# Performance work log

Hardware: AMD Instinct MI355X
Metric: run time of the kernel (lower is better)

Reference implementation:

```python
import jax, jax.numpy as jnp
import numpy as np

N = 50000
E = 800000
IN_DIM = 512
HID = 256
LAT = 128
K = 10
ALPHA = 0.1
BN_EPS = 1e-5


def setup_inputs() -> dict:
    key = jax.random.key(0)
    ks = jax.random.split(key, 6)
    x = jax.random.normal(ks[0], (N, IN_DIM), dtype=jnp.float32)
    edge_index = jax.random.randint(ks[1], (2, E), 0, N, dtype=jnp.int64)
    W_proj = jax.random.normal(ks[2], (IN_DIM, LAT), dtype=jnp.float32) * (IN_DIM ** -0.5)
    W1 = jax.random.normal(ks[3], (LAT, HID), dtype=jnp.float32) * (LAT ** -0.5)
    W2 = jax.random.normal(ks[4], (HID, LAT), dtype=jnp.float32) * (HID ** -0.5)
    return {
        "x": x, "edge_index": edge_index, "W_proj": W_proj,
        "W1": W1, "b1": jnp.zeros((HID,), jnp.float32),
        "gamma1": jnp.ones((HID,), jnp.float32), "beta1": jnp.zeros((HID,), jnp.float32),
        "mean1": jnp.zeros((HID,), jnp.float32), "var1": jnp.ones((HID,), jnp.float32),
        "W2": W2, "b2": jnp.zeros((LAT,), jnp.float32),
        "gamma2": jnp.ones((LAT,), jnp.float32), "beta2": jnp.zeros((LAT,), jnp.float32),
        "mean2": jnp.zeros((LAT,), jnp.float32), "var2": jnp.ones((LAT,), jnp.float32),
    }


def _gcn_norm(edge_index, n):
    # add self-loops, symmetric normalization D^-1/2 A D^-1/2 (PyG gcn_norm)
    loops = jnp.arange(n, dtype=edge_index.dtype)
    src = jnp.concatenate([edge_index[0], loops])
    dst = jnp.concatenate([edge_index[1], loops])
    deg = jax.ops.segment_sum(jnp.ones_like(dst, jnp.float32), dst, num_segments=n)
    dinv = jax.lax.rsqrt(jnp.maximum(deg, 1.0))  # deg >= 1 with self-loops
    norm = dinv[src] * dinv[dst]
    return src, dst, norm


def _propagate(h, src, dst, norm, n):
    # gather -> scale -> scatter-add: out[dst] += norm * h[src]
    return jax.ops.segment_sum(h[src] * norm[:, None], dst, num_segments=n)


def _bn(h, gamma, beta, mean, var):
    # BatchNorm1d in eval mode (running stats)
    return (h - mean) * jax.lax.rsqrt(var + BN_EPS) * gamma + beta


def reference(x, edge_index, W_proj, W1, b1, gamma1, beta1, mean1, var1,
              W2, b2, gamma2, beta2, mean2, var2):
    n = x.shape[0]
    src, dst, norm = _gcn_norm(edge_index, n)

    z0 = x @ W_proj                                   # [N, LAT]
    h1 = _propagate(z0 @ W1, src, dst, norm, n) + b1  # GCNConv 1
    h1 = jax.nn.relu(_bn(h1, gamma1, beta1, mean1, var1))
    h2 = _propagate(h1 @ W2, src, dst, norm, n) + b2  # GCNConv 2
    h2 = jax.nn.relu(_bn(h2, gamma2, beta2, mean2, var2))

    # APPNP: h_k = (1-alpha) * A_hat h_{k-1} + alpha * h_0
    def step(h, _):
        h = (1.0 - ALPHA) * _propagate(h, src, dst, norm, n) + ALPHA * h2
        return h, None
    z_refined, _ = jax.lax.scan(step, h2, None, length=K)

    z = z_refined + z0
    row, col = edge_index[0], edge_index[1]
    adj = jax.nn.sigmoid(jnp.sum(z[row] * z[col], axis=1))  # [E]
    return adj, z
```

## Files before the change

kernel.cpp:

```cpp
#include <hip/hip_runtime.h>

#define N_NODES 50000
#define N_EDGES 800000
#define IN_DIM  512
#define HID     256
#define LAT     128
#define K_ITERS 10
#define BN_EPS  1e-5f

typedef __attribute__((ext_vector_type(8))) short bf16x8;
typedef __attribute__((ext_vector_type(4))) float f32x4;

__device__ inline float bflo(unsigned v) { return __builtin_bit_cast(float, v << 16); }
__device__ inline float bfhi(unsigned v) { return __builtin_bit_cast(float, v & 0xffff0000u); }
__device__ inline unsigned f2bf_bits(float f)
{
    unsigned u = __builtin_bit_cast(unsigned, f);
    return (u + 0x7fffu + ((u >> 16) & 1u)) >> 16;
}
__device__ inline unsigned packbf(float x, float y)
{
    return f2bf_bits(x) | (f2bf_bits(y) << 16);
}

__global__ void detect_dtype_kernel(const int* __restrict__ ei32, int* __restrict__ flag)
{
    __shared__ int any;
    if (threadIdx.x == 0) any = 0;
    __syncthreads();
    int local = 0;
    for (int i = threadIdx.x; i < 4096; i += blockDim.x)
        local |= ei32[2 * i + 1];
    if (local) atomicOr(&any, 1);
    __syncthreads();
    if (threadIdx.x == 0) flag[0] = (any != 0) ? 1 : 0;
}

__global__ void init_cnt_kernel(int* __restrict__ cnt, int n)
{
    int i = blockIdx.x * blockDim.x + threadIdx.x;
    if (i < n) cnt[i] = 1;
}

__global__ void convert_count_kernel(const void* __restrict__ ei, const int* __restrict__ flag,
                                     int* __restrict__ srcE, int* __restrict__ dstE,
                                     int* __restrict__ cnt, int E)
{
    int e = blockIdx.x * blockDim.x + threadIdx.x;
    if (e >= E) return;
    int s, d;
    if (*flag) {
        const int* p = (const int*)ei;
        s = p[e]; d = p[E + e];
    } else {
        const long long* p = (const long long*)ei;
        s = (int)p[e]; d = (int)p[E + e];
    }
    srcE[e] = s;
    dstE[e] = d;
    atomicAdd(&cnt[d], 1);
}

__global__ __launch_bounds__(256) void block_sum_kernel(const int* __restrict__ cnt,
                                                        int* __restrict__ bsum, int n)
{
    __shared__ int s[256];
    int i = blockIdx.x * 256 + threadIdx.x;
    s[threadIdx.x] = (i < n) ? cnt[i] : 0;
    __syncthreads();
    for (int off = 128; off > 0; off >>= 1) {
        if (threadIdx.x < off) s[threadIdx.x] += s[threadIdx.x + off];
        __syncthreads();
    }
    if (threadIdx.x == 0) bsum[blockIdx.x] = s[0];
}

__global__ __launch_bounds__(256) void block_scan_kernel(int* __restrict__ bsum, int nb)
{
    __shared__ int s[256];
    int t = threadIdx.x;
    int v = (t < nb) ? bsum[t] : 0;
    s[t] = v;
    __syncthreads();
    for (int off = 1; off < 256; off <<= 1) {
        int u = (t >= off) ? s[t - off] : 0;
        __syncthreads();
        s[t] += u;
        __syncthreads();
    }
    if (t < nb) bsum[t] = s[t] - v;
}

__global__ __launch_bounds__(256) void final_scan_kernel(const int* __restrict__ cnt,
                                                         const int* __restrict__ bsum,
                                                         int* __restrict__ rowoff,
                                                         int* __restrict__ cursor,
                                                         float* __restrict__ dinv, int n)
{
    __shared__ int s[256];
    int t = threadIdx.x;
    int i = blockIdx.x * 256 + t;
    int c = (i < n) ? cnt[i] : 0;
    s[t] = c;
    __syncthreads();
    for (int off = 1; off < 256; off <<= 1) {
        int u = (t >= off) ? s[t - off] : 0;
        __syncthreads();
        s[t] += u;
        __syncthreads();
    }
    if (i < n) {
        int excl = bsum[blockIdx.x] + s[t] - c;
        rowoff[i] = excl;
        cursor[i] = excl;
        dinv[i] = rsqrtf((float)c);
    }
    if (i == 0) rowoff[n] = N_EDGES + N_NODES;
}

__global__ void scatter_kernel(const int* __restrict__ srcE, const int* __restrict__ dstE,
                               const float* __restrict__ dinv, int* __restrict__ cursor,
                               uint2* __restrict__ csr, int E, int n)
{
    int e = blockIdx.x * blockDim.x + threadIdx.x;
    if (e >= E + n) return;
    int s, d;
    if (e < E) { s = srcE[e]; d = dstE[e]; }
    else       { s = e - E;   d = s; }
    int pos = atomicAdd(&cursor[d], 1);
    float w = dinv[s] * dinv[d];
    csr[pos] = make_uint2((unsigned)s, __builtin_bit_cast(unsigned, w));
}

__global__ void transpose_cvt_kernel(const float* __restrict__ in, unsigned short* __restrict__ out,
                                     int R, int C)
{
    int idx = blockIdx.x * 256 + threadIdx.x;
    if (idx >= R * C) return;
    int c = idx / R, r = idx - c * R;
    out[idx] = (unsigned short)f2bf_bits(in[r * C + c]);
}

template<int KDIM, int EPI, bool AF32>
__global__ __launch_bounds__(256) void gemm_pipe(const void* __restrict__ Ain,
                                                 const unsigned short* __restrict__ Bt,
                                                 unsigned short* __restrict__ Cout,
                                                 int M, int Nc,
                                                 const float* __restrict__ cb,
                                                 const float* __restrict__ cg,
                                                 const float* __restrict__ cbe,
                                                 const float* __restrict__ cm,
                                                 const float* __restrict__ cv)
{
    constexpr int NK = KDIM / 32;
    constexpr int PREF = AF32 ? (NK < 4 ? NK : 4) : (NK < 8 ? NK : 8);
    const int wave = threadIdx.x >> 6;
    const int lane = threadIdx.x & 63;
    const int s  = lane & 15;
    const int kc = lane >> 4;
    const int wrow0   = blockIdx.y * 64 + wave * 16;
    const int colbase = blockIdx.x * 128;
    int arow = wrow0 + s; if (arow > M - 1) arow = M - 1;

    const float*          Af = (const float*)Ain + (size_t)arow * KDIM + 8 * kc;
    const unsigned short* Ah = (const unsigned short*)Ain + (size_t)arow * KDIM + 8 * kc;
    const unsigned short* Bp = Bt + (size_t)(colbase + s) * KDIM + 8 * kc;

    float4 Araw[AF32 ? PREF : 1][2];
    bf16x8 Areg[AF32 ? 1 : PREF];
    bf16x8 Breg[2][8];
    f32x4  acc[8] = {};

#pragma unroll
    for (int i = 0; i < PREF; ++i) {
        if constexpr (AF32) {
            Araw[i][0] = *(const float4*)(Af + 32 * i);
            Araw[i][1] = *(const float4*)(Af + 32 * i + 4);
        } else {
            Areg[i] = *(const bf16x8*)(Ah + 32 * i);
        }
    }
#pragma unroll
    for (int t = 0; t < 8; ++t)
        Breg[0][t] = *(const bf16x8*)(Bp + (size_t)16 * t * KDIM);

#pragma unroll
    for (int k = 0; k < NK; ++k) {
        if (k + 1 < NK) {
#pragma unroll
            for (int t = 0; t < 8; ++t)
                Breg[(k + 1) & 1][t] = *(const bf16x8*)(Bp + (size_t)16 * t * KDIM + 32 * (k + 1));
        }
        bf16x8 af;
        if constexpr (AF32) {
            float4 u0 = Araw[k % PREF][0];
            float4 u1 = Araw[k % PREF][1];
            if (k + PREF < NK) {
                Araw[k % PREF][0] = *(const float4*)(Af + 32 * (k + PREF));
                Araw[k % PREF][1] = *(const float4*)(Af + 32 * (k + PREF) + 4);
            }
            af[0] = (short)f2bf_bits(u0.x); af[1] = (short)f2bf_bits(u0.y);
            af[2] = (short)f2bf_bits(u0.z); af[3] = (short)f2bf_bits(u0.w);
            af[4] = (short)f2bf_bits(u1.x); af[5] = (short)f2bf_bits(u1.y);
            af[6] = (short)f2bf_bits(u1.z); af[7] = (short)f2bf_bits(u1.w);
        } else {
            af = Areg[k % PREF];
            if (k + PREF < NK)
                Areg[k % PREF] = *(const bf16x8*)(Ah + 32 * (k + PREF));
        }
#pragma unroll
        for (int t = 0; t < 8; ++t)
            acc[t] = __builtin_amdgcn_mfma_f32_16x16x32_bf16(af, Breg[k & 1][t], acc[t], 0, 0, 0);
    }

#pragma unroll
    for (int t = 0; t < 8; ++t) {
        const int col = colbase + t * 16 + s;
        float sc = 1.f, sh = 0.f;
        if (EPI == 1) {
            sc = cg[col] * rsqrtf(cv[col] + BN_EPS);
            sh = (cb[col] - cm[col]) * sc + cbe[col];
        }
#pragma unroll
        for (int j = 0; j < 4; ++j) {
            const int crow = wrow0 + kc * 4 + j;
            if (crow < M) {
                float xv = acc[t][j];
                if (EPI == 1) xv = fmaxf(fmaf(xv, sc, sh), 0.f);
                Cout[(size_t)crow * Nc + col] = (unsigned short)f2bf_bits(xv);
            }
        }
    }
}

template<int MODE>
__global__ __launch_bounds__(256) void prop_row(const unsigned* __restrict__ in,
                                                const int* __restrict__ rowoff,
                                                const unsigned long long* __restrict__ csr,
                                                const unsigned* __restrict__ h2h,
                                                const unsigned* __restrict__ z0h,
                                                float* __restrict__ outf,
                                                unsigned* __restrict__ outh,
                                                const float* __restrict__ bb,
                                                const float* __restrict__ bg,
                                                const float* __restrict__ bbe,
                                                const float* __restrict__ bm,
                                                const float* __restrict__ bv)
{
    const int node = blockIdx.x * 4 + (threadIdx.x >> 6);
    const int lane = threadIdx.x & 63;
    const int g = lane >> 4, s = lane & 15;
    const int e0 = rowoff[node], e1 = rowoff[node + 1];

    float f[8] = {};
    int e = e0 + g;
    while (e < e1) {
        unsigned long long P[6];
        uint4 V[6];
#pragma unroll
        for (int i = 0; i < 6; ++i) { P[i] = 0; V[i] = make_uint4(0u, 0u, 0u, 0u); }
#pragma unroll
        for (int i = 0; i < 6; ++i)
            if (e + 4 * i < e1) P[i] = csr[e + 4 * i];
#pragma unroll
        for (int i = 0; i < 6; ++i)
            if (e + 4 * i < e1) V[i] = *(const uint4*)&in[(size_t)(unsigned)P[i] * 64 + 4 * s];
#pragma unroll
        for (int i = 0; i < 6; ++i) {
            const float w = __builtin_bit_cast(float, (unsigned)(P[i] >> 32));
            f[0] = fmaf(w, bflo(V[i].x), f[0]); f[1] = fmaf(w, bfhi(V[i].x), f[1]);
            f[2] = fmaf(w, bflo(V[i].y), f[2]); f[3] = fmaf(w, bfhi(V[i].y), f[3]);
            f[4] = fmaf(w, bflo(V[i].z), f[4]); f[5] = fmaf(w, bfhi(V[i].z), f[5]);
            f[6] = fmaf(w, bflo(V[i].w), f[6]); f[7] = fmaf(w, bfhi(V[i].w), f[7]);
        }
        e += 24;
    }
#pragma unroll
    for (int i = 0; i < 8; ++i) {
        f[i] += __shfl_xor(f[i], 16, 64);
        f[i] += __shfl_xor(f[i], 32, 64);
    }

    if (g == 0) {
        const size_t o = (size_t)node * 64 + 4 * s;
        uint4 ov;
        if (MODE == 0) {
            ov.x = packbf(f[0], f[1]); ov.y = packbf(f[2], f[3]);
            ov.z = packbf(f[4], f[5]); ov.w = packbf(f[6], f[7]);
            *(uint4*)&outh[o] = ov;
        } else if (MODE == 1) {
            float4 G0 = *(const float4*)&bg[8 * s],  G1 = *(const float4*)&bg[8 * s + 4];
            float4 V0 = *(const float4*)&bv[8 * s],  V1 = *(const float4*)&bv[8 * s + 4];
            float4 B0 = *(const float4*)&bb[8 * s],  B1 = *(const float4*)&bb[8 * s + 4];
            float4 M0 = *(const float4*)&bm[8 * s],  M1 = *(const float4*)&bm[8 * s + 4];
            float4 E0 = *(const float4*)&bbe[8 * s], E1 = *(const float4*)&bbe[8 * s + 4];
            float gg[8] = {G0.x, G0.y, G0.z, G0.w, G1.x, G1.y, G1.z, G1.w};
            float vv[8] = {V0.x, V0.y, V0.z, V0.w, V1.x, V1.y, V1.z, V1.w};
            float bbv[8] = {B0.x, B0.y, B0.z, B0.w, B1.x, B1.y, B1.z, B1.w};
            float mm[8] = {M0.x, M0.y, M0.z, M0.w, M1.x, M1.y, M1.z, M1.w};
            float ee[8] = {E0.x, E0.y, E0.z, E0.w, E1.x, E1.y, E1.z, E1.w};
            float r[8];
#pragma unroll
            for (int i = 0; i < 8; ++i) {
                float sc = gg[i] * rsqrtf(vv[i] + BN_EPS);
                float sh = (bbv[i] - mm[i]) * sc + ee[i];
                r[i] = fmaxf(fmaf(f[i], sc, sh), 0.f);
            }
            ov.x = packbf(r[0], r[1]); ov.y = packbf(r[2], r[3]);
            ov.z = packbf(r[4], r[5]); ov.w = packbf(r[6], r[7]);
            *(uint4*)&outh[o] = ov;
        } else if (MODE == 2) {
            uint4 hv = *(const uint4*)&h2h[o];
            ov.x = packbf(fmaf(0.9f, f[0], 0.1f * bflo(hv.x)), fmaf(0.9f, f[1], 0.1f * bfhi(hv.x)));
            ov.y = packbf(fmaf(0.9f, f[2], 0.1f * bflo(hv.y)), fmaf(0.9f, f[3], 0.1f * bfhi(hv.y)));
            ov.z = packbf(fmaf(0.9f, f[4], 0.1f * bflo(hv.z)), fmaf(0.9f, f[5], 0.1f * bfhi(hv.z)));
            ov.w = packbf(fmaf(0.9f, f[6], 0.1f * bflo(hv.w)), fmaf(0.9f, f[7], 0.1f * bfhi(hv.w)));
            *(uint4*)&outh[o] = ov;
        } else {
            uint4 hv = *(const uint4*)&h2h[o];
            uint4 zv = *(const uint4*)&z0h[o];
            float r[8];
            r[0] = fmaf(0.9f, f[0], 0.1f * bflo(hv.x)) + bflo(zv.x);
            r[1] = fmaf(0.9f, f[1], 0.1f * bfhi(hv.x)) + bfhi(zv.x);
            r[2] = fmaf(0.9f, f[2], 0.1f * bflo(hv.y)) + bflo(zv.y);
            r[3] = fmaf(0.9f, f[3], 0.1f * bfhi(hv.y)) + bfhi(zv.y);
            r[4] = fmaf(0.9f, f[4], 0.1f * bflo(hv.z)) + bflo(zv.z);
            r[5] = fmaf(0.9f, f[5], 0.1f * bfhi(hv.z)) + bfhi(zv.z);
            r[6] = fmaf(0.9f, f[6], 0.1f * bflo(hv.w)) + bflo(zv.w);
            r[7] = fmaf(0.9f, f[7], 0.1f * bfhi(hv.w)) + bfhi(zv.w);
            *(float4*)&outf[(size_t)node * LAT + 8 * s]     = make_float4(r[0], r[1], r[2], r[3]);
            *(float4*)&outf[(size_t)node * LAT + 8 * s + 4] = make_float4(r[4], r[5], r[6], r[7]);
            ov.x = packbf(r[0], r[1]); ov.y = packbf(r[2], r[3]);
            ov.z = packbf(r[4], r[5]); ov.w = packbf(r[6], r[7]);
            *(uint4*)&outh[o] = ov;
        }
    }
}

__global__ __launch_bounds__(256) void edge_dot_mfma(const unsigned* __restrict__ zh,
                                                     const int* __restrict__ srcE,
                                                     const int* __restrict__ dstE,
                                                     float* __restrict__ adj)
{
    const int gw = blockIdx.x * 4 + (threadIdx.x >> 6);
    const int base = gw * 16;
    const int lane = threadIdx.x & 63;
    const int s = lane & 15, kc = lane >> 4;
    const int r = srcE[base + s];
    const int c = dstE[base + s];
    const unsigned* zr = &zh[(size_t)r * 64 + 4 * kc];
    const unsigned* zc = &zh[(size_t)c * 64 + 4 * kc];
    f32x4 acc = {};
#pragma unroll
    for (int k0 = 0; k0 < 4; ++k0) {
        bf16x8 af = *(const bf16x8*)(zr + 16 * k0);
        bf16x8 bf = *(const bf16x8*)(zc + 16 * k0);
        acc = __builtin_amdgcn_mfma_f32_16x16x32_bf16(af, bf, acc, 0, 0, 0);
    }
    if ((s >> 2) == kc) {
        const int j = s & 3;
        float v = (j == 0) ? acc[0] : (j == 1) ? acc[1] : (j == 2) ? acc[2] : acc[3];
        adj[base + s] = 1.f / (1.f + expf(-v));
    }
}

extern "C" void kernel_launch(void* const* d_in, const int* in_sizes, int n_in,
                              void* d_out, int out_size, void* d_ws, size_t ws_size,
                              hipStream_t stream)
{
    const float* x     = (const float*)d_in[0];
    const void*  ei    = d_in[1];
    const float* Wproj = (const float*)d_in[2];
    const float* W1    = (const float*)d_in[3];
    const float* b1    = (const float*)d_in[4];
    const float* g1    = (const float*)d_in[5];
    const float* be1   = (const float*)d_in[6];
    const float* m1    = (const float*)d_in[7];
    const float* v1    = (const float*)d_in[8];
    const float* W2    = (const float*)d_in[9];
    const float* b2    = (const float*)d_in[10];
    const float* g2    = (const float*)d_in[11];
    const float* be2   = (const float*)d_in[12];
    const float* m2    = (const float*)d_in[13];
    const float* v2    = (const float*)d_in[14];

    float* out_adj = (float*)d_out;
    float* out_z   = (float*)d_out + N_EDGES;

    char* w = (char*)d_ws;
    size_t off = 0;
    auto alloc = [&](size_t bytes) {
        void* p = w + off;
        off += (bytes + 255) & ~(size_t)255;
        return p;
    };
    const size_t NB = (size_t)N_NODES * 64 * 4;
    const int NBLK = (N_NODES + 255) / 256;

    int*            flag   = (int*)           alloc(4);
    int*            cnt    = (int*)           alloc((size_t)N_NODES * 4);
    int*            cursor = (int*)           alloc((size_t)N_NODES * 4);
    int*            rowoff = (int*)           alloc((size_t)(N_NODES + 1) * 4);
    float*          dinv   = (float*)         alloc((size_t)N_NODES * 4);
    int*            bsum   = (int*)           alloc(256 * 4);
    int*            srcE   = (int*)           alloc((size_t)N_EDGES * 4);
    int*            dstE   = (int*)           alloc((size_t)N_EDGES * 4);
    uint2*          csr    = (uint2*)         alloc((size_t)(N_EDGES + N_NODES) * 8);
    unsigned short* Wpt    = (unsigned short*)alloc((size_t)LAT * IN_DIM * 2);
    unsigned short* W1t    = (unsigned short*)alloc((size_t)HID * LAT * 2);
    unsigned short* W2t    = (unsigned short*)alloc((size_t)LAT * HID * 2);
    unsigned*       z0h    = (unsigned*)      alloc(NB);
    unsigned*       p0h    = (unsigned*)      alloc(NB);
    unsigned short* h1h    = (unsigned short*)alloc(2 * NB);
    unsigned*       t2h    = (unsigned*)      alloc(NB);
    unsigned*       h2h    = (unsigned*)      alloc(NB);

    unsigned* pingA = (unsigned*)h1h;
    unsigned* pingB = (unsigned*)h1h + N_NODES * 64;

    detect_dtype_kernel<<<1, 256, 0, stream>>>((const int*)ei, flag);
    init_cnt_kernel<<<(N_NODES + 255) / 256, 256, 0, stream>>>(cnt, N_NODES);
    convert_count_kernel<<<(N_EDGES + 255) / 256, 256, 0, stream>>>(ei, flag, srcE, dstE, cnt, N_EDGES);
    block_sum_kernel<<<NBLK, 256, 0, stream>>>(cnt, bsum, N_NODES);
    block_scan_kernel<<<1, 256, 0, stream>>>(bsum, NBLK);
    final_scan_kernel<<<NBLK, 256, 0, stream>>>(cnt, bsum, rowoff, cursor, dinv, N_NODES);
    scatter_kernel<<<(N_EDGES + N_NODES + 255) / 256, 256, 0, stream>>>(srcE, dstE, dinv, cursor,
                                                                        csr, N_EDGES, N_NODES);

    transpose_cvt_kernel<<<(IN_DIM * LAT + 255) / 256, 256, 0, stream>>>(Wproj, Wpt, IN_DIM, LAT);
    transpose_cvt_kernel<<<(LAT * HID + 255) / 256, 256, 0, stream>>>(W1, W1t, LAT, HID);
    transpose_cvt_kernel<<<(HID * LAT + 255) / 256, 256, 0, stream>>>(W2, W2t, HID, LAT);

    const int gy = (N_NODES + 63) / 64;
    const int pgrid = N_NODES / 4;

    gemm_pipe<IN_DIM, 0, true><<<dim3(1, gy), 256, 0, stream>>>(x, Wpt, (unsigned short*)z0h,
                                                                N_NODES, LAT,
                                                                nullptr, nullptr, nullptr, nullptr, nullptr);
    prop_row<0><<<pgrid, 256, 0, stream>>>(z0h, rowoff, (const unsigned long long*)csr,
                                           nullptr, nullptr, nullptr, p0h,
                                           nullptr, nullptr, nullptr, nullptr, nullptr);
    gemm_pipe<LAT, 1, false><<<dim3(2, gy), 256, 0, stream>>>(p0h, W1t, h1h, N_NODES, HID,
                                                              b1, g1, be1, m1, v1);
    gemm_pipe<HID, 0, false><<<dim3(1, gy), 256, 0, stream>>>(h1h, W2t, (unsigned short*)t2h,
                                                              N_NODES, LAT,
                                                              nullptr, nullptr, nullptr, nullptr, nullptr);
    prop_row<1><<<pgrid, 256, 0, stream>>>(t2h, rowoff, (const unsigned long long*)csr,
                                           nullptr, nullptr, nullptr, h2h,
                                           b2, g2, be2, m2, v2);

    const unsigned* cur = h2h;
    for (int it = 0; it < K_ITERS; ++it) {
        if (it == K_ITERS - 1) {
            prop_row<3><<<pgrid, 256, 0, stream>>>(cur, rowoff, (const unsigned long long*)csr,
                                                   h2h, z0h, out_z, z0h,
                                                   nullptr, nullptr, nullptr, nullptr, nullptr);
        } else {
            unsigned* nxt = (it & 1) ? pingB : pingA;
            prop_row<2><<<pgrid, 256, 0, stream>>>(cur, rowoff, (const unsigned long long*)csr,
                                                   h2h, nullptr, nullptr, nxt,
                                                   nullptr, nullptr, nullptr, nullptr, nullptr);
            cur = nxt;
        }
    }

    edge_dot_mfma<<<N_EDGES / 64, 256, 0, stream>>>(z0h, srcE, dstE, out_adj);
}
```

Baseline: 719.7 us.

## Stage weight tiles in LDS for GEMMs with MFMA-friendly pre-tiled layout

The GEMM kernels now stage 64-deep chunks of the weight matrix into shared memory with a register double-buffered prefetch, so B is read once per block instead of every wave reading it from global memory. The weight transpose kernel writes a tiled layout that lets each thread copy contiguous 64-byte runs and lets the MFMA operand reads come straight from LDS. This targets redundant global/L2 traffic for B in the dense projections. In exchange it adds block-wide barriers per chunk and LDS bank-access patterns that may reduce overlap.

```diff
diff --git a/kernel.cpp b/kernel.cpp
--- a/kernel.cpp
+++ b/kernel.cpp
@@ -132,85 +132,107 @@
     csr[pos] = make_uint2((unsigned)s, __builtin_bit_cast(unsigned, w));
 }
 
-__global__ void transpose_cvt_kernel(const float* __restrict__ in, unsigned short* __restrict__ out,
-                                     int R, int C)
+__global__ void transpose_cvt_tile(const float* __restrict__ in, unsigned short* __restrict__ out,
+                                   int K, int C)
 {
     int idx = blockIdx.x * 256 + threadIdx.x;
-    if (idx >= R * C) return;
-    int c = idx / R, r = idx - c * R;
-    out[idx] = (unsigned short)f2bf_bits(in[r * C + c]);
+    if (idx >= K * C) return;
+    int k = idx / C, col = idx - k * C;
+    int dst = (col >> 7) * (K * 128) + (k >> 3) * 1024 + ((col & 127) << 3) + (k & 7);
+    out[dst] = (unsigned short)f2bf_bits(in[idx]);
 }
 
 template<int KDIM, int EPI, bool AF32>
-__global__ __launch_bounds__(256) void gemm_pipe(const void* __restrict__ Ain,
-                                                 const unsigned short* __restrict__ Bt,
-                                                 unsigned short* __restrict__ Cout,
-                                                 int M, int Nc,
-                                                 const float* __restrict__ cb,
-                                                 const float* __restrict__ cg,
-                                                 const float* __restrict__ cbe,
-                                                 const float* __restrict__ cm,
-                                                 const float* __restrict__ cv)
-{
-    constexpr int NK = KDIM / 32;
-    constexpr int PREF = AF32 ? (NK < 4 ? NK : 4) : (NK < 8 ? NK : 8);
-    const int wave = threadIdx.x >> 6;
-    const int lane = threadIdx.x & 63;
+__global__ __launch_bounds__(256) void gemm_lds(const void* __restrict__ Ain,
+                                                const unsigned short* __restrict__ Bt,
+                                                unsigned short* __restrict__ Cout,
+                                                int M, int Nc,
+                                                const float* __restrict__ cb,
+                                                const float* __restrict__ cg,
+                                                const float* __restrict__ cbe,
+                                                const float* __restrict__ cm,
+                                                const float* __restrict__ cv)
+{
+    constexpr int BK = 64;
+    constexpr int NC = KDIM / BK;
+    __shared__ unsigned short Bl[BK * 128];
+    const int tid  = threadIdx.x;
+    const int wave = tid >> 6;
+    const int lane = tid & 63;
     const int s  = lane & 15;
     const int kc = lane >> 4;
     const int wrow0   = blockIdx.y * 64 + wave * 16;
     const int colbase = blockIdx.x * 128;
     int arow = wrow0 + s; if (arow > M - 1) arow = M - 1;
 
-    const float*          Af = (const float*)Ain + (size_t)arow * KDIM + 8 * kc;
-    const unsigned short* Ah = (const unsigned short*)Ain + (size_t)arow * KDIM + 8 * kc;
-    const unsigned short* Bp = Bt + (size_t)(colbase + s) * KDIM + 8 * kc;
-
-    float4 Araw[AF32 ? PREF : 1][2];
-    bf16x8 Areg[AF32 ? 1 : PREF];
-    bf16x8 Breg[2][8];
+    const float*          Af   = (const float*)Ain + (size_t)arow * KDIM + 8 * kc;
+    const unsigned short* Ahp  = (const unsigned short*)Ain + (size_t)arow * KDIM + 8 * kc;
+    const unsigned short* Bblk = Bt + (size_t)blockIdx.x * KDIM * 128;
+
+    float4 Arf[2][2][2];
+    bf16x8 Arh[2][2];
+    uint4  Bst[4];
     f32x4  acc[8] = {};
 
-#pragma unroll
-    for (int i = 0; i < PREF; ++i) {
+    {
+        const uint4* src = (const uint4*)(Bblk + tid * 32);
+        Bst[0] = src[0]; Bst[1] = src[1]; Bst[2] = src[2]; Bst[3] = src[3];
+    }
+#pragma unroll
+    for (int kk = 0; kk < 2; ++kk) {
         if constexpr (AF32) {
-            Araw[i][0] = *(const float4*)(Af + 32 * i);
-            Araw[i][1] = *(const float4*)(Af + 32 * i + 4);
+            Arf[0][kk][0] = *(const float4*)(Af + 32 * kk);
+            Arf[0][kk][1] = *(const float4*)(Af + 32 * kk + 4);
         } else {
-            Areg[i] = *(const bf16x8*)(Ah + 32 * i);
-        }
-    }
-#pragma unroll
-    for (int t = 0; t < 8; ++t)
-        Breg[0][t] = *(const bf16x8*)(Bp + (size_t)16 * t * KDIM);
-
-#pragma unroll
-    for (int k = 0; k < NK; ++k) {
-        if (k + 1 < NK) {
-#pragma unroll
-            for (int t = 0; t < 8; ++t)
-                Breg[(k + 1) & 1][t] = *(const bf16x8*)(Bp + (size_t)16 * t * KDIM + 32 * (k + 1));
-        }
-        bf16x8 af;
-        if constexpr (AF32) {
-            float4 u0 = Araw[k % PREF][0];
-            float4 u1 = Araw[k % PREF][1];
-            if (k + PREF < NK) {
-                Araw[k % PREF][0] = *(const float4*)(Af + 32 * (k + PREF));
-                Araw[k % PREF][1] = *(const float4*)(Af + 32 * (k + PREF) + 4);
+            Arh[0][kk] = *(const bf16x8*)(Ahp + 32 * kk);
+        }
+    }
+    {
+        uint4* d = (uint4*)&Bl[tid * 32];
+        d[0] = Bst[0]; d[1] = Bst[1]; d[2] = Bst[2]; d[3] = Bst[3];
+    }
+    __syncthreads();
+
+#pragma unroll
+    for (int c = 0; c < NC; ++c) {
+        if (c + 1 < NC) {
+            const uint4* src = (const uint4*)(Bblk + (c + 1) * 8192 + tid * 32);
+            Bst[0] = src[0]; Bst[1] = src[1]; Bst[2] = src[2]; Bst[3] = src[3];
+#pragma unroll
+            for (int kk = 0; kk < 2; ++kk) {
+                if constexpr (AF32) {
+                    Arf[(c + 1) & 1][kk][0] = *(const float4*)(Af + (c + 1) * 64 + 32 * kk);
+                    Arf[(c + 1) & 1][kk][1] = *(const float4*)(Af + (c + 1) * 64 + 32 * kk + 4);
+                } else {
+                    Arh[(c + 1) & 1][kk] = *(const bf16x8*)(Ahp + (c + 1) * 64 + 32 * kk);
+                }
             }
-            af[0] = (short)f2bf_bits(u0.x); af[1] = (short)f2bf_bits(u0.y);
-            af[2] = (short)f2bf_bits(u0.z); af[3] = (short)f2bf_bits(u0.w);
-            af[4] = (short)f2bf_bits(u1.x); af[5] = (short)f2bf_bits(u1.y);
-            af[6] = (short)f2bf_bits(u1.z); af[7] = (short)f2bf_bits(u1.w);
-        } else {
-            af = Areg[k % PREF];
-            if (k + PREF < NK)
-                Areg[k % PREF] = *(const bf16x8*)(Ah + 32 * (k + PREF));
-        }
-#pragma unroll
-        for (int t = 0; t < 8; ++t)
-            acc[t] = __builtin_amdgcn_mfma_f32_16x16x32_bf16(af, Breg[k & 1][t], acc[t], 0, 0, 0);
+        }
+#pragma unroll
+        for (int kk = 0; kk < 2; ++kk) {
+            bf16x8 af;
+            if constexpr (AF32) {
+                float4 u0 = Arf[c & 1][kk][0];
+                float4 u1 = Arf[c & 1][kk][1];
+                af[0] = (short)f2bf_bits(u0.x); af[1] = (short)f2bf_bits(u0.y);
+                af[2] = (short)f2bf_bits(u0.z); af[3] = (short)f2bf_bits(u0.w);
+                af[4] = (short)f2bf_bits(u1.x); af[5] = (short)f2bf_bits(u1.y);
+                af[6] = (short)f2bf_bits(u1.z); af[7] = (short)f2bf_bits(u1.w);
+            } else {
+                af = Arh[c & 1][kk];
+            }
+#pragma unroll
+            for (int t = 0; t < 8; ++t) {
+                bf16x8 bf = *(const bf16x8*)&Bl[((kk * 4 + kc) * 128 + t * 16 + s) * 8];
+                acc[t] = __builtin_amdgcn_mfma_f32_16x16x32_bf16(af, bf, acc[t], 0, 0, 0);
+            }
+        }
+        __syncthreads();
+        if (c + 1 < NC) {
+            uint4* d = (uint4*)&Bl[tid * 32];
+            d[0] = Bst[0]; d[1] = Bst[1]; d[2] = Bst[2]; d[3] = Bst[3];
+            __syncthreads();
+        }
     }
 
 #pragma unroll
@@ -427,24 +449,24 @@
     scatter_kernel<<<(N_EDGES + N_NODES + 255) / 256, 256, 0, stream>>>(srcE, dstE, dinv, cursor,
                                                                         csr, N_EDGES, N_NODES);
 
-    transpose_cvt_kernel<<<(IN_DIM * LAT + 255) / 256, 256, 0, stream>>>(Wproj, Wpt, IN_DIM, LAT);
-    transpose_cvt_kernel<<<(LAT * HID + 255) / 256, 256, 0, stream>>>(W1, W1t, LAT, HID);
-    transpose_cvt_kernel<<<(HID * LAT + 255) / 256, 256, 0, stream>>>(W2, W2t, HID, LAT);
+    transpose_cvt_tile<<<(IN_DIM * LAT + 255) / 256, 256, 0, stream>>>(Wproj, Wpt, IN_DIM, LAT);
+    transpose_cvt_tile<<<(LAT * HID + 255) / 256, 256, 0, stream>>>(W1, W1t, LAT, HID);
+    transpose_cvt_tile<<<(HID * LAT + 255) / 256, 256, 0, stream>>>(W2, W2t, HID, LAT);
 
     const int gy = (N_NODES + 63) / 64;
     const int pgrid = N_NODES / 4;
 
-    gemm_pipe<IN_DIM, 0, true><<<dim3(1, gy), 256, 0, stream>>>(x, Wpt, (unsigned short*)z0h,
-                                                                N_NODES, LAT,
-                                                                nullptr, nullptr, nullptr, nullptr, nullptr);
+    gemm_lds<IN_DIM, 0, true><<<dim3(1, gy), 256, 0, stream>>>(x, Wpt, (unsigned short*)z0h,
+                                                               N_NODES, LAT,
+                                                               nullptr, nullptr, nullptr, nullptr, nullptr);
     prop_row<0><<<pgrid, 256, 0, stream>>>(z0h, rowoff, (const unsigned long long*)csr,
                                            nullptr, nullptr, nullptr, p0h,
                                            nullptr, nullptr, nullptr, nullptr, nullptr);
-    gemm_pipe<LAT, 1, false><<<dim3(2, gy), 256, 0, stream>>>(p0h, W1t, h1h, N_NODES, HID,
-                                                              b1, g1, be1, m1, v1);
-    gemm_pipe<HID, 0, false><<<dim3(1, gy), 256, 0, stream>>>(h1h, W2t, (unsigned short*)t2h,
-                                                              N_NODES, LAT,
-                                                              nullptr, nullptr, nullptr, nullptr, nullptr);
+    gemm_lds<LAT, 1, false><<<dim3(2, gy), 256, 0, stream>>>(p0h, W1t, h1h, N_NODES, HID,
+                                                             b1, g1, be1, m1, v1);
+    gemm_lds<HID, 0, false><<<dim3(1, gy), 256, 0, stream>>>(h1h, W2t, (unsigned short*)t2h,
+                                                             N_NODES, LAT,
+                                                             nullptr, nullptr, nullptr, nullptr, nullptr);
     prop_row<1><<<pgrid, 256, 0, stream>>>(t2h, rowoff, (const unsigned long long*)csr,
                                            nullptr, nullptr, nullptr, h2h,
                                            b2, g2, be2, m2, v2);
```

After: 680.2 us. -5.5%, faster.
